# Kernel optimization log

Measured on AMD Instinct MI355X. Metric: run time of the kernel, lower is better.

Reference implementation:

```python
import math
import jax, jax.numpy as jnp
import numpy as np

B, S, E, H = 1, 2048, 2048, 16
QL, KL = 1536, 512          # q_lora_rank, kv_lora_rank
DN, DR, DV = 128, 64, 128   # qk_nope_head_dim, qk_rope_head_dim, v_head_dim
DQ = DN + DR                # q_head_dim = 192
ROPE_BASE = 10000.0
EPS = 1e-6


def _rope_cache(seq_len):
    # YaRN with scaling_factor=1.0 reduces exactly to standard RoPE (freq_extra == freq_inter,
    # mscale ratio == 1), matching DeepseekV2YarnRotaryEmbedding at default settings.
    inv_freq = 1.0 / (ROPE_BASE ** (np.arange(0, DR, 2, dtype=np.float32) / DR))
    t = np.arange(seq_len, dtype=np.float32)
    freqs = np.outer(t, inv_freq)
    emb = np.concatenate([freqs, freqs], axis=-1)  # (S, DR)
    return jnp.asarray(np.cos(emb)), jnp.asarray(np.sin(emb))


def _rmsnorm(x, w):
    return x * jax.lax.rsqrt(jnp.mean(x * x, axis=-1, keepdims=True) + EPS) * w


def _apply_rope(x, cos, sin):
    # x: (B, S, H, D). DeepseekV2 apply_rotary_pos_emb first de-interleaves
    # (view(..., d//2, 2).transpose) then uses rotate_half.
    b, s, h, d = x.shape
    xr = x.reshape(b, s, h, d // 2, 2)
    x = jnp.concatenate([xr[..., 0], xr[..., 1]], axis=-1)  # de-interleave
    rot = jnp.concatenate([-x[..., d // 2:], x[..., : d // 2]], axis=-1)
    return x * cos[None, :, None, :] + rot * sin[None, :, None, :]


def setup_inputs() -> dict:
    key = jax.random.key(0)
    ks = jax.random.split(key, 8)
    w = lambda k, shape, fan_in: (jax.random.normal(k, shape, jnp.float32) / math.sqrt(fan_in))
    return {
        "x": jax.random.normal(ks[0], (B, S, E), jnp.float32),
        "w_q_a": w(ks[1], (E, QL), E),
        "q_a_ln": jnp.ones((QL,), jnp.float32),
        "w_q_b": w(ks[2], (QL, H * DQ), QL),
        "w_kv_a": w(ks[3], (E, KL + DR), E),
        "kv_a_ln": jnp.ones((KL,), jnp.float32),
        "w_kv_b": w(ks[4], (KL, H * (DN + DV)), KL),
        "w_out": w(ks[5], (H * DV, E), H * DV),
    }


def reference(x, w_q_a, q_a_ln, w_q_b, w_kv_a, kv_a_ln, w_kv_b, w_out):
    b, s, _ = x.shape
    # Q: low-rank down-proj -> RMSNorm -> up-proj, split nope/rope parts
    q = (_rmsnorm(x @ w_q_a, q_a_ln) @ w_q_b).reshape(b, s, H, DQ)
    q_nope, q_pe = q[..., :DN], q[..., DN:]
    # KV: joint compressed latent + shared (MQA-style) rope key
    ckv = x @ w_kv_a                         # (b, s, KL+DR)
    c_kv, k_pe = ckv[..., :KL], ckv[..., KL:]
    kv = (_rmsnorm(c_kv, kv_a_ln) @ w_kv_b).reshape(b, s, H, DN + DV)
    k_nope, v = kv[..., :DN], kv[..., DN:]
    # Partial RoPE on the 64-dim rope slice only
    cos, sin = _rope_cache(s)
    q_pe = _apply_rope(q_pe, cos, sin)
    k_pe = _apply_rope(k_pe.reshape(b, s, 1, DR), cos, sin)
    qf = jnp.concatenate([q_nope, q_pe], axis=-1)                       # (b,s,H,192)
    kf = jnp.concatenate([k_nope, jnp.broadcast_to(k_pe, (b, s, H, DR))], axis=-1)
    # Causal softmax attention, scale = 1/sqrt(q_head_dim)
    scale = 1.0 / math.sqrt(DQ)
    scores = jnp.einsum("bqhd,bkhd->bhqk", qf, kf) * scale
    mask = jnp.tril(jnp.ones((s, s), dtype=bool))
    scores = jnp.where(mask[None, None], scores, jnp.finfo(scores.dtype).min)
    p = jax.nn.softmax(scores, axis=-1)
    o = jnp.einsum("bhqk,bkhd->bqhd", p, v).reshape(b, s, H * DV)
    return o @ w_out
```

## Files before the change

kernel.cpp:

```cpp
#include <hip/hip_runtime.h>
#include <hip/hip_bf16.h>
#include <math.h>

#define SS   2048
#define EE   2048
#define HH   16
#define QLAT 1536
#define KLAT 512
#define DN   128
#define DR   64
#define DV   128
#define DQ   192
#define KVD  256
#define CKVW 576
#define QW   3072
#define KVW  4096
#define OW   2048
#define QAC  2112

#define NSEG 4
#define PT_STRIDE 72
#define KTSZ (6 * 64 * 32)

typedef __attribute__((ext_vector_type(8))) short short8;
typedef __attribute__((ext_vector_type(4))) float f32x4;

__global__ void detect_dtype(const unsigned int* __restrict__ lnw, int* flag) {
    *flag = (lnw[0] == 0x3F803F80u) ? 1 : 0;
}

__device__ __forceinline__ float ld_in(const void* p, size_t i, int bf) {
    if (bf) return __bfloat162float(((const __hip_bfloat16*)p)[i]);
    return ((const float*)p)[i];
}

__device__ __forceinline__ ushort f2b(float v) {
    __hip_bfloat16 b = __float2bfloat16(v);
    return *(ushort*)&b;
}
__device__ __forceinline__ float b2f(ushort u) {
    __hip_bfloat16 b = *(__hip_bfloat16*)&u;
    return __bfloat162float(b);
}

__device__ __forceinline__ void async16(const ushort* g, ushort* l) {
    __builtin_amdgcn_global_load_lds(
        (const __attribute__((address_space(1))) void*)g,
        (__attribute__((address_space(3))) void*)l, 16, 0, 0);
}

__global__ __launch_bounds__(256) void conv_x_bf(
    const void* __restrict__ src, ushort* __restrict__ dst, int n, const int* flag) {
    const int bf = *flag;
    int i = (blockIdx.x * 256 + threadIdx.x) * 4;
    if (i >= n) return;
    ushort4 u;
    u.x = f2b(ld_in(src, i + 0, bf));
    u.y = f2b(ld_in(src, i + 1, bf));
    u.z = f2b(ld_in(src, i + 2, bf));
    u.w = f2b(ld_in(src, i + 3, bf));
    *(ushort4*)(dst + i) = u;
}

__global__ __launch_bounds__(256) void transpose_bf(
    const void* __restrict__ in, ushort* __restrict__ out,
    int R, int C, const int* flag) {
    const int bf = *flag;
    __shared__ ushort t[64][66];
    const int c0 = blockIdx.x * 64, r0 = blockIdx.y * 64;
    const int lane = threadIdx.x & 63, grp = threadIdx.x >> 6;
    #pragma unroll
    for (int p = 0; p < 16; ++p) {
        int r = p * 4 + grp;
        t[lane][r] = f2b(ld_in(in, (size_t)(r0 + r) * C + c0 + lane, bf));
    }
    __syncthreads();
    const int ro = (threadIdx.x & 31) * 2, co = threadIdx.x >> 5;
    #pragma unroll
    for (int p = 0; p < 8; ++p) {
        int c = p * 8 + co;
        ushort2 u = *(const ushort2*)&t[c][ro];
        *(ushort2*)&out[(size_t)(c0 + c) * R + r0 + ro] = u;
    }
}

__global__ __launch_bounds__(256) void gemm_bf(
    const ushort* __restrict__ A, const ushort* __restrict__ Bt,
    void* __restrict__ C, int N, int K, int lda, int ldb, int ldc,
    int cmode, const int* __restrict__ cflag) {
    __shared__ ushort As[128 * 32];
    __shared__ ushort Bs[128 * 32];
    const int tid = threadIdx.x;
    const int bm = blockIdx.y * 128, bn = blockIdx.x * 128;
    const int lane = tid & 63, wv = tid >> 6;
    const int wm = (wv & 1) * 64, wn = (wv >> 1) * 64;
    const int ln = lane & 15, quad = lane >> 4;

    f32x4 acc[4][4];
    #pragma unroll
    for (int i = 0; i < 4; ++i)
        #pragma unroll
        for (int j = 0; j < 4; ++j) acc[i][j] = (f32x4){0.f, 0.f, 0.f, 0.f};

    const int srow = tid >> 2;
    const int spart = (((tid & 3) ^ ((tid >> 3) & 3))) * 8;
    const ushort* Ag0 = A  + (size_t)(bm + srow) * lda + spart;
    const ushort* Ag1 = Ag0 + (size_t)64 * lda;
    const ushort* Bg0 = Bt + (size_t)(bn + srow) * ldb + spart;
    const ushort* Bg1 = Bg0 + (size_t)64 * ldb;
    ushort* Asl = As + tid * 8;
    ushort* Bsl = Bs + tid * 8;
    const bool bok0 = (bn + srow) < N;
    const bool bok1 = (bn + 64 + srow) < N;
    const int swq = (quad ^ ((ln >> 1) & 3)) * 8;

    for (int k0 = 0; k0 < K; k0 += 32) {
        async16(Ag0 + k0, Asl);
        async16(Ag1 + k0, Asl + 2048);
        if (bok0) async16(Bg0 + k0, Bsl);
        if (bok1) async16(Bg1 + k0, Bsl + 2048);
        __syncthreads();
        short8 af[4], bfr[4];
        #pragma unroll
        for (int t = 0; t < 4; ++t) {
            af[t]  = *(const short8*)&As[(wm + t * 16 + ln) * 32 + swq];
            bfr[t] = *(const short8*)&Bs[(wn + t * 16 + ln) * 32 + swq];
        }
        #pragma unroll
        for (int i = 0; i < 4; ++i)
            #pragma unroll
            for (int j = 0; j < 4; ++j)
                acc[i][j] = __builtin_amdgcn_mfma_f32_16x16x32_bf16(af[i], bfr[j], acc[i][j], 0, 0, 0);
        __syncthreads();
    }

    const int cbf = (cmode == 2) ? *cflag : cmode;
    #pragma unroll
    for (int i = 0; i < 4; ++i) {
        #pragma unroll
        for (int r = 0; r < 4; ++r) {
            const int m = bm + wm + i * 16 + quad * 4 + r;
            #pragma unroll
            for (int j = 0; j < 4; ++j) {
                const int n = bn + wn + j * 16 + ln;
                if (n < N) {
                    if (cbf) ((ushort*)C)[(size_t)m * ldc + n] = f2b(acc[i][j][r]);
                    else     ((float*)C)[(size_t)m * ldc + n] = acc[i][j][r];
                }
            }
        }
    }
}

__global__ __launch_bounds__(256) void gemm_bf64(
    const ushort* __restrict__ A, const ushort* __restrict__ Bt,
    void* __restrict__ C, int N, int K, int lda, int ldb, int ldc,
    int cmode, const int* __restrict__ cflag) {
    __shared__ ushort As[64 * 32];
    __shared__ ushort Bs[128 * 32];
    const int tid = threadIdx.x;
    const int bm = blockIdx.y * 64, bn = blockIdx.x * 128;
    const int lane = tid & 63, wv = tid >> 6;
    const int wm = (wv & 1) * 32, wn = (wv >> 1) * 64;
    const int ln = lane & 15, quad = lane >> 4;

    f32x4 acc[2][4];
    #pragma unroll
    for (int i = 0; i < 2; ++i)
        #pragma unroll
        for (int j = 0; j < 4; ++j) acc[i][j] = (f32x4){0.f, 0.f, 0.f, 0.f};

    const int srow = tid >> 2;
    const int spart = (((tid & 3) ^ ((tid >> 3) & 3))) * 8;
    const ushort* Ag0 = A  + (size_t)(bm + srow) * lda + spart;
    const ushort* Bg0 = Bt + (size_t)(bn + srow) * ldb + spart;
    const ushort* Bg1 = Bg0 + (size_t)64 * ldb;
    ushort* Asl = As + tid * 8;
    ushort* Bsl = Bs + tid * 8;
    const bool bok0 = (bn + srow) < N;
    const bool bok1 = (bn + 64 + srow) < N;
    const int swq = (quad ^ ((ln >> 1) & 3)) * 8;

    for (int k0 = 0; k0 < K; k0 += 32) {
        async16(Ag0 + k0, Asl);
        if (bok0) async16(Bg0 + k0, Bsl);
        if (bok1) async16(Bg1 + k0, Bsl + 2048);
        __syncthreads();
        short8 af[2], bfr[4];
        #pragma unroll
        for (int t = 0; t < 2; ++t)
            af[t] = *(const short8*)&As[(wm + t * 16 + ln) * 32 + swq];
        #pragma unroll
        for (int t = 0; t < 4; ++t)
            bfr[t] = *(const short8*)&Bs[(wn + t * 16 + ln) * 32 + swq];
        #pragma unroll
        for (int i = 0; i < 2; ++i)
            #pragma unroll
            for (int j = 0; j < 4; ++j)
                acc[i][j] = __builtin_amdgcn_mfma_f32_16x16x32_bf16(af[i], bfr[j], acc[i][j], 0, 0, 0);
        __syncthreads();
    }

    const int cbf = (cmode == 2) ? *cflag : cmode;
    #pragma unroll
    for (int i = 0; i < 2; ++i) {
        #pragma unroll
        for (int r = 0; r < 4; ++r) {
            const int m = bm + wm + i * 16 + quad * 4 + r;
            #pragma unroll
            for (int j = 0; j < 4; ++j) {
                const int n = bn + wn + j * 16 + ln;
                if (n < N) {
                    if (cbf) ((ushort*)C)[(size_t)m * ldc + n] = f2b(acc[i][j][r]);
                    else     ((float*)C)[(size_t)m * ldc + n] = acc[i][j][r];
                }
            }
        }
    }
}

__global__ __launch_bounds__(256) void rmsnorm_bf(
    ushort* __restrict__ x, const void* __restrict__ w,
    int cols, int stride, const int* wflag) {
    const int wbf = *wflag;
    ushort* p = x + (size_t)blockIdx.x * stride;
    float ss = 0.f;
    for (int i = threadIdx.x; i < cols; i += 256) { float v = b2f(p[i]); ss += v * v; }
    #pragma unroll
    for (int off = 32; off; off >>= 1) ss += __shfl_xor(ss, off);
    __shared__ float red[4];
    const int wid = threadIdx.x >> 6, lane = threadIdx.x & 63;
    if (lane == 0) red[wid] = ss;
    __syncthreads();
    const float tot = red[0] + red[1] + red[2] + red[3];
    const float scale = rsqrtf(tot / (float)cols + 1e-6f);
    for (int i = threadIdx.x; i < cols; i += 256)
        p[i] = f2b(b2f(p[i]) * scale * ld_in(w, i, wbf));
}

__device__ __forceinline__ void rope64(const float* in, float t, float* out) {
    #pragma unroll
    for (int i = 0; i < 32; ++i) {
        float inv = powf(10000.0f, -(float)i / 32.0f);
        float sv, cv;
        sincosf(t * inv, &sv, &cv);
        float x0 = in[2 * i], x1 = in[2 * i + 1];
        out[i]      = x0 * cv - x1 * sv;
        out[i + 32] = x1 * cv + x0 * sv;
    }
}

__global__ void rope_q_bf(ushort* __restrict__ q) {
    int idx = blockIdx.x * blockDim.x + threadIdx.x;
    if (idx >= SS * HH) return;
    int s = idx >> 4, h = idx & 15;
    ushort* p = q + (size_t)s * QW + h * DQ + DN;
    float buf[DR], out[DR];
    #pragma unroll
    for (int i = 0; i < DR; ++i) buf[i] = b2f(p[i]);
    rope64(buf, (float)s, out);
    #pragma unroll
    for (int i = 0; i < DR; ++i) p[i] = f2b(out[i]);
}

__global__ void rope_k_bf(const ushort* __restrict__ ckv, ushort* __restrict__ kpe,
                          int stride) {
    int s = blockIdx.x * blockDim.x + threadIdx.x;
    if (s >= SS) return;
    const ushort* p = ckv + (size_t)s * stride + KLAT;
    float buf[DR], out[DR];
    #pragma unroll
    for (int i = 0; i < DR; ++i) buf[i] = b2f(p[i]);
    rope64(buf, (float)s, out);
    ushort* dp = kpe + (size_t)s * DR;
    #pragma unroll
    for (int i = 0; i < DR; ++i) dp[i] = f2b(out[i]);
}

__global__ __launch_bounds__(256) void build_kf(
    const ushort* __restrict__ kv, const ushort* __restrict__ kpe,
    ushort* __restrict__ kf) {
    int idx = blockIdx.x * 256 + threadIdx.x;
    int part = idx % 24;
    int rest = idx / 24;
    int h = rest & 15, s = rest >> 4;
    short8 v;
    if (part < 16) v = *(const short8*)(kv + (size_t)s * KVW + h * KVD + part * 8);
    else           v = *(const short8*)(kpe + (size_t)s * DR + (part - 16) * 8);
    *(short8*)(kf + ((size_t)h * SS + s) * 192 + part * 8) = v;
}

__global__ __launch_bounds__(256) void build_vt2(
    const ushort* __restrict__ kv, ushort* __restrict__ vt2) {
    __shared__ ushort Vl[64 * 136];
    const int ck = blockIdx.x, h = blockIdx.y;
    const int tid = threadIdx.x;
    const int lane = tid & 63, wv = tid >> 6;
    #pragma unroll
    for (int rr = 0; rr < 4; ++rr) {
        int n = rr * 256 + tid;
        int key = n >> 4, part = n & 15;
        short8 v = *(const short8*)(kv + (size_t)(ck * 64 + key) * KVW + h * KVD + DN + part * 8);
        *(short8*)&Vl[key * 136 + part * 8] = v;
    }
    __syncthreads();
    const int ln = lane & 15, quad = lane >> 4;
    ushort* dst = vt2 + (((size_t)h * 32 + ck) * 16) * 512;
    #pragma unroll
    for (int w = 0; w < 4; ++w) {
        int idx2 = wv * 4 + w;
        int kb2 = idx2 >> 3, nb = idx2 & 7;
        short8 v;
        #pragma unroll
        for (int j = 0; j < 8; ++j)
            ((ushort*)&v)[j] = Vl[(kb2 * 32 + quad * 8 + j) * 136 + nb * 16 + ln];
        *(short8*)(dst + (size_t)idx2 * 512 + lane * 8) = v;
    }
}

__global__ __launch_bounds__(256, 2) void attn_mfma2(
    const ushort* __restrict__ qbf, const ushort* __restrict__ kf,
    const ushort* __restrict__ vt2, ushort* __restrict__ opart,
    float* __restrict__ ml) {
    const int seg = blockIdx.x, bq = 31 - blockIdx.y, h = blockIdx.z;
    const int ctot = bq + 1;
    const int c_lo = (seg * ctot) >> 2;
    const int nch = (((seg + 1) * ctot) >> 2) - c_lo;
    if (nch <= 0) return;

    __shared__ ushort Kt[2 * KTSZ];
    __shared__ ushort Pt[4][16 * PT_STRIDE];

    const int tid = threadIdx.x, lane = tid & 63, wl = tid >> 6;
    const int ln = lane & 15, quad = lane >> 4;
    const int qw = bq * 64 + wl * 16;
    const int kstart = c_lo << 6;
    const float scale = 0.07216878364870322f;

    short8 aq[6];
    const ushort* qrow = qbf + (size_t)(qw + ln) * QW + h * DQ;
    #pragma unroll
    for (int kb = 0; kb < 6; ++kb)
        aq[kb] = *(const short8*)(qrow + kb * 32 + quad * 8);

    const ushort* kfh = kf + (size_t)h * SS * 192;
    const ushort* vth2 = vt2 + ((size_t)h * 32 * 16) * 512 + lane * 8;

    const int key_s = tid >> 2;
    const int swp = ((tid & 3) ^ ((tid >> 3) & 3)) * 8;
    const ushort* kg = kfh + (size_t)(kstart + key_s) * 192 + swp;
    const int swq = (quad ^ ((ln >> 1) & 3)) * 8;

    f32x4 oacc[8];
    #pragma unroll
    for (int f = 0; f < 8; ++f) oacc[f] = (f32x4){0.f, 0.f, 0.f, 0.f};
    float mrow[4] = {-INFINITY, -INFINITY, -INFINITY, -INFINITY};
    float lrow[4] = {0.f, 0.f, 0.f, 0.f};

    {
        ushort* kd = Kt + tid * 8;
        #pragma unroll
        for (int i = 0; i < 6; ++i)
            async16(kg + i * 32, kd + i * 2048);
        kg += (size_t)64 * 192;
    }

    for (int c = 0; c < nch; ++c) {
        const int k0 = kstart + (c << 6);
        asm volatile("s_waitcnt vmcnt(0)" ::: "memory");
        __builtin_amdgcn_s_barrier();
        asm volatile("" ::: "memory");
        if (c + 1 < nch) {
            ushort* kd = Kt + ((c + 1) & 1) * KTSZ + tid * 8;
            #pragma unroll
            for (int i = 0; i < 6; ++i)
                async16(kg + i * 32, kd + i * 2048);
            kg += (size_t)64 * 192;
        }
        const ushort* Kcur = Kt + (c & 1) * KTSZ;

        const ushort* vfr = vth2 + (size_t)(k0 >> 6) * 16 * 512;
        short8 bv0[8];
        #pragma unroll
        for (int nb = 0; nb < 8; ++nb)
            bv0[nb] = *(const short8*)(vfr + (size_t)nb * 512);
        f32x4 s[4];
        #pragma unroll
        for (int ns = 0; ns < 4; ++ns) s[ns] = (f32x4){0.f, 0.f, 0.f, 0.f};
        __builtin_amdgcn_s_setprio(1);
        #pragma unroll
        for (int ns = 0; ns < 4; ++ns)
            #pragma unroll
            for (int kb = 0; kb < 6; ++kb) {
                short8 bk = *(const short8*)&Kcur[(kb * 64 + ns * 16 + ln) * 32 + swq];
                s[ns] = __builtin_amdgcn_mfma_f32_16x16x32_bf16(aq[kb], bk, s[ns], 0, 0, 0);
            }
        __builtin_amdgcn_s_setprio(0);
        float pv[4][4], rmax[4];
        #pragma unroll
        for (int r = 0; r < 4; ++r) rmax[r] = -1e30f;
        #pragma unroll
        for (int ns = 0; ns < 4; ++ns)
            #pragma unroll
            for (int r = 0; r < 4; ++r) {
                int key = k0 + ns * 16 + ln;
                int qr = qw + quad * 4 + r;
                float v = s[ns][r] * scale;
                if (key > qr) v = -1e30f;
                pv[ns][r] = v;
                rmax[r] = fmaxf(rmax[r], v);
            }
        #pragma unroll
        for (int off = 8; off; off >>= 1)
            #pragma unroll
            for (int r = 0; r < 4; ++r)
                rmax[r] = fmaxf(rmax[r], __shfl_xor(rmax[r], off));
        float alpha[4], psum[4];
        #pragma unroll
        for (int r = 0; r < 4; ++r) {
            float mnew = fmaxf(mrow[r], rmax[r]);
            alpha[r] = __expf(mrow[r] - mnew);
            mrow[r] = mnew;
        }
        #pragma unroll
        for (int ns = 0; ns < 4; ++ns)
            #pragma unroll
            for (int r = 0; r < 4; ++r)
                pv[ns][r] = __expf(pv[ns][r] - mrow[r]);
        #pragma unroll
        for (int r = 0; r < 4; ++r)
            psum[r] = (pv[0][r] + pv[1][r]) + (pv[2][r] + pv[3][r]);
        #pragma unroll
        for (int off = 8; off; off >>= 1)
            #pragma unroll
            for (int r = 0; r < 4; ++r)
                psum[r] += __shfl_xor(psum[r], off);
        #pragma unroll
        for (int r = 0; r < 4; ++r) lrow[r] = lrow[r] * alpha[r] + psum[r];
        #pragma unroll
        for (int f = 0; f < 8; ++f)
            #pragma unroll
            for (int r = 0; r < 4; ++r) oacc[f][r] *= alpha[r];
        #pragma unroll
        for (int ns = 0; ns < 4; ++ns)
            #pragma unroll
            for (int r = 0; r < 4; ++r)
                Pt[wl][(quad * 4 + r) * PT_STRIDE + ns * 16 + ln] = f2b(pv[ns][r]);
        short8 bv1[8];
        #pragma unroll
        for (int nb = 0; nb < 8; ++nb)
            bv1[nb] = *(const short8*)(vfr + (size_t)(8 + nb) * 512);
        short8 pa0 = *(const short8*)&Pt[wl][ln * PT_STRIDE + quad * 8];
        short8 pa1 = *(const short8*)&Pt[wl][ln * PT_STRIDE + 32 + quad * 8];
        __builtin_amdgcn_s_setprio(1);
        #pragma unroll
        for (int nb = 0; nb < 8; ++nb)
            oacc[nb] = __builtin_amdgcn_mfma_f32_16x16x32_bf16(pa0, bv0[nb], oacc[nb], 0, 0, 0);
        #pragma unroll
        for (int nb = 0; nb < 8; ++nb)
            oacc[nb] = __builtin_amdgcn_mfma_f32_16x16x32_bf16(pa1, bv1[nb], oacc[nb], 0, 0, 0);
        __builtin_amdgcn_s_setprio(0);
    }

    const size_t pbase = (((size_t)h * 32 + bq) * NSEG + seg) * 64;
    #pragma unroll
    for (int nb = 0; nb < 8; ++nb)
        #pragma unroll
        for (int r = 0; r < 4; ++r)
            opart[(pbase + wl * 16 + quad * 4 + r) * 128 + nb * 16 + ln] = f2b(oacc[nb][r]);
    if (ln == 0) {
        #pragma unroll
        for (int r = 0; r < 4; ++r) {
            ml[(pbase + wl * 16 + quad * 4 + r) * 2]     = mrow[r];
            ml[(pbase + wl * 16 + quad * 4 + r) * 2 + 1] = lrow[r];
        }
    }
}

__global__ __launch_bounds__(256) void merge_attn(
    const ushort* __restrict__ opart, const float* __restrict__ ml,
    ushort* __restrict__ obf) {
    const int q = blockIdx.x;
    const int bq = q >> 6, row = q & 63;
    const int ctot = bq + 1;
    const int t = threadIdx.x;
    #pragma unroll
    for (int pp = 0; pp < 8; ++pp) {
        int idx = pp * 256 + t;
        int h = idx >> 7, d = idx & 127;
        size_t rbase = (((size_t)h * 32 + bq) * NSEG) * 64 + row;
        float M = -1e30f;
        #pragma unroll
        for (int s = 0; s < NSEG; ++s) {
            if ((((s + 1) * ctot) >> 2) > ((s * ctot) >> 2))
                M = fmaxf(M, ml[(rbase + (size_t)s * 64) * 2]);
        }
        float L = 0.f, acc = 0.f;
        #pragma unroll
        for (int s = 0; s < NSEG; ++s) {
            if ((((s + 1) * ctot) >> 2) > ((s * ctot) >> 2)) {
                size_t ri = rbase + (size_t)s * 64;
                float w = __expf(ml[ri * 2] - M);
                L += w * ml[ri * 2 + 1];
                acc += w * b2f(opart[ri * 128 + d]);
            }
        }
        obf[(size_t)q * OW + h * DV + d] = f2b(acc / L);
    }
}

extern "C" void kernel_launch(void* const* d_in, const int* in_sizes, int n_in,
                              void* d_out, int out_size, void* d_ws, size_t ws_size,
                              hipStream_t stream) {
    const void* x       = d_in[0];
    const void* w_q_a   = d_in[1];
    const void* q_a_ln  = d_in[2];
    const void* w_q_b   = d_in[3];
    const void* w_kv_a  = d_in[4];
    const void* kv_a_ln = d_in[5];
    const void* w_kv_b  = d_in[6];
    const void* w_out   = d_in[7];

    char* ws = (char*)d_ws;
    int*    flag  = (int*)ws;
    ushort* qbf   = (ushort*)(ws + 256);
    ushort* obf   = qbf   + (size_t)SS * QW;
    ushort* wqat  = obf   + (size_t)SS * OW;
    ushort* wkvat = wqat  + (size_t)QLAT * EE;
    ushort* wqbt  = wkvat + (size_t)CKVW * EE;
    ushort* wkvbt = wqbt  + (size_t)QW * QLAT;
    ushort* woutt = wkvbt + (size_t)KVW * KLAT;
    ushort* kf    = woutt + (size_t)EE * OW;
    ushort* vt2   = kf    + (size_t)HH * SS * 192;
    float*  ml    = (float*)(vt2 + (size_t)HH * SS * DV);
    ushort* qac   = (ushort*)(ml + (size_t)HH * 32 * NSEG * 64 * 2);
    ushort* xbf   = qac   + (size_t)SS * QAC;
    ushort* kvbf  = xbf   + (size_t)SS * EE;
    ushort* kpebf = kvbf  + (size_t)SS * KVW;
    ushort* opart = qac;

    detect_dtype<<<1, 1, 0, stream>>>((const unsigned int*)q_a_ln, flag);

    conv_x_bf<<<(SS * EE / 4 + 255) / 256, 256, 0, stream>>>(x, xbf, SS * EE, flag);
    transpose_bf<<<dim3(QLAT / 64, EE / 64), 256, 0, stream>>>(w_q_a, wqat, EE, QLAT, flag);
    transpose_bf<<<dim3(CKVW / 64, EE / 64), 256, 0, stream>>>(w_kv_a, wkvat, EE, CKVW, flag);
    transpose_bf<<<dim3(QW / 64, QLAT / 64), 256, 0, stream>>>(w_q_b, wqbt, QLAT, QW, flag);
    transpose_bf<<<dim3(KVW / 64, KLAT / 64), 256, 0, stream>>>(w_kv_b, wkvbt, KLAT, KVW, flag);
    transpose_bf<<<dim3(EE / 64, OW / 64), 256, 0, stream>>>(w_out, woutt, OW, EE, flag);

    gemm_bf64<<<dim3((QAC + 127) / 128, SS / 64), 256, 0, stream>>>(
        xbf, wqat, qac, QAC, EE, EE, EE, QAC, 1, nullptr);

    rmsnorm_bf<<<SS, 256, 0, stream>>>(qac, q_a_ln, QLAT, QAC, flag);
    rmsnorm_bf<<<SS, 256, 0, stream>>>(qac + QLAT, kv_a_ln, KLAT, QAC, flag);

    gemm_bf<<<dim3(QW / 128, SS / 128), 256, 0, stream>>>(
        qac, wqbt, qbf, QW, QLAT, QAC, QLAT, QW, 1, nullptr);
    gemm_bf<<<dim3(KVW / 128, SS / 128), 256, 0, stream>>>(
        qac + QLAT, wkvbt, kvbf, KVW, KLAT, QAC, KLAT, KVW, 1, nullptr);

    rope_q_bf<<<(SS * HH + 255) / 256, 256, 0, stream>>>(qbf);
    rope_k_bf<<<(SS + 63) / 64, 64, 0, stream>>>(qac + QLAT, kpebf, QAC);

    build_kf<<<SS * HH * 24 / 256, 256, 0, stream>>>(kvbf, kpebf, kf);
    build_vt2<<<dim3(SS / 64, HH), 256, 0, stream>>>(kvbf, vt2);

    attn_mfma2<<<dim3(NSEG, SS / 64, HH), 256, 0, stream>>>(qbf, kf, vt2, opart, ml);
    merge_attn<<<SS, 256, 0, stream>>>(opart, ml, obf);

    gemm_bf64<<<dim3(EE / 128, SS / 64), 256, 0, stream>>>(
        obf, woutt, d_out, EE, OW, OW, OW, EE, 2, flag);
}
```

Before: 440.8 us.

## Double-buffer GEMM LDS loads and merge transpose, rmsnorm and rope launches

Both bf16 MFMA GEMM kernels now use two LDS buffers. The async global-to-LDS loads for the next K-step are issued while MFMAs run on the current step, which removes one barrier per iteration and raises wave priority around the MFMA block. Separately, the five weight-transpose launches are merged into one 3D-grid kernel, the two RMSNorm launches into one, and the q/k RoPE launches into one, to cut launch overhead. The trade-off is doubled LDS per GEMM block, which may lower occupancy, plus some idle blocks in the merged transpose grid.

```diff
diff --git a/kernel.cpp b/kernel.cpp
--- a/kernel.cpp
+++ b/kernel.cpp
@@ -62,12 +62,26 @@
     *(ushort4*)(dst + i) = u;
 }
 
-__global__ __launch_bounds__(256) void transpose_bf(
-    const void* __restrict__ in, ushort* __restrict__ out,
-    int R, int C, const int* flag) {
+__global__ __launch_bounds__(256) void transpose5_bf(
+    const void* __restrict__ s0, const void* __restrict__ s1,
+    const void* __restrict__ s2, const void* __restrict__ s3,
+    const void* __restrict__ s4,
+    ushort* __restrict__ d0, ushort* __restrict__ d1, ushort* __restrict__ d2,
+    ushort* __restrict__ d3, ushort* __restrict__ d4,
+    const int* flag) {
+    const int z = blockIdx.z;
+    const void* in; ushort* out; int R, C;
+    switch (z) {
+        case 0:  in = s0; out = d0; R = EE;   C = QLAT; break;
+        case 1:  in = s1; out = d1; R = EE;   C = CKVW; break;
+        case 2:  in = s2; out = d2; R = QLAT; C = QW;   break;
+        case 3:  in = s3; out = d3; R = KLAT; C = KVW;  break;
+        default: in = s4; out = d4; R = OW;   C = EE;   break;
+    }
+    const int c0 = blockIdx.x * 64, r0 = blockIdx.y * 64;
+    if (c0 >= C || r0 >= R) return;
     const int bf = *flag;
     __shared__ ushort t[64][66];
-    const int c0 = blockIdx.x * 64, r0 = blockIdx.y * 64;
     const int lane = threadIdx.x & 63, grp = threadIdx.x >> 6;
     #pragma unroll
     for (int p = 0; p < 16; ++p) {
@@ -88,8 +102,8 @@
     const ushort* __restrict__ A, const ushort* __restrict__ Bt,
     void* __restrict__ C, int N, int K, int lda, int ldb, int ldc,
     int cmode, const int* __restrict__ cflag) {
-    __shared__ ushort As[128 * 32];
-    __shared__ ushort Bs[128 * 32];
+    __shared__ ushort As[2][128 * 32];
+    __shared__ ushort Bs[2][128 * 32];
     const int tid = threadIdx.x;
     const int bm = blockIdx.y * 128, bn = blockIdx.x * 128;
     const int lane = tid & 63, wv = tid >> 6;
@@ -108,30 +122,49 @@
     const ushort* Ag1 = Ag0 + (size_t)64 * lda;
     const ushort* Bg0 = Bt + (size_t)(bn + srow) * ldb + spart;
     const ushort* Bg1 = Bg0 + (size_t)64 * ldb;
-    ushort* Asl = As + tid * 8;
-    ushort* Bsl = Bs + tid * 8;
     const bool bok0 = (bn + srow) < N;
     const bool bok1 = (bn + 64 + srow) < N;
     const int swq = (quad ^ ((ln >> 1) & 3)) * 8;
-
-    for (int k0 = 0; k0 < K; k0 += 32) {
-        async16(Ag0 + k0, Asl);
-        async16(Ag1 + k0, Asl + 2048);
-        if (bok0) async16(Bg0 + k0, Bsl);
-        if (bok1) async16(Bg1 + k0, Bsl + 2048);
-        __syncthreads();
+    const int nsteps = K >> 5;
+
+    {
+        ushort* Asl = As[0] + tid * 8;
+        ushort* Bsl = Bs[0] + tid * 8;
+        async16(Ag0, Asl);
+        async16(Ag1, Asl + 2048);
+        if (bok0) async16(Bg0, Bsl);
+        if (bok1) async16(Bg1, Bsl + 2048);
+    }
+
+    for (int c = 0; c < nsteps; ++c) {
+        asm volatile("s_waitcnt vmcnt(0)" ::: "memory");
+        __builtin_amdgcn_s_barrier();
+        asm volatile("" ::: "memory");
+        if (c + 1 < nsteps) {
+            const int k1 = (c + 1) << 5;
+            const int nb = (c + 1) & 1;
+            ushort* Asl = As[nb] + tid * 8;
+            ushort* Bsl = Bs[nb] + tid * 8;
+            async16(Ag0 + k1, Asl);
+            async16(Ag1 + k1, Asl + 2048);
+            if (bok0) async16(Bg0 + k1, Bsl);
+            if (bok1) async16(Bg1 + k1, Bsl + 2048);
+        }
+        const ushort* Ac = As[c & 1];
+        const ushort* Bc = Bs[c & 1];
         short8 af[4], bfr[4];
         #pragma unroll
         for (int t = 0; t < 4; ++t) {
-            af[t]  = *(const short8*)&As[(wm + t * 16 + ln) * 32 + swq];
-            bfr[t] = *(const short8*)&Bs[(wn + t * 16 + ln) * 32 + swq];
-        }
+            af[t]  = *(const short8*)&Ac[(wm + t * 16 + ln) * 32 + swq];
+            bfr[t] = *(const short8*)&Bc[(wn + t * 16 + ln) * 32 + swq];
+        }
+        __builtin_amdgcn_s_setprio(1);
         #pragma unroll
         for (int i = 0; i < 4; ++i)
             #pragma unroll
             for (int j = 0; j < 4; ++j)
                 acc[i][j] = __builtin_amdgcn_mfma_f32_16x16x32_bf16(af[i], bfr[j], acc[i][j], 0, 0, 0);
-        __syncthreads();
+        __builtin_amdgcn_s_setprio(0);
     }
 
     const int cbf = (cmode == 2) ? *cflag : cmode;
@@ -156,8 +189,8 @@
     const ushort* __restrict__ A, const ushort* __restrict__ Bt,
     void* __restrict__ C, int N, int K, int lda, int ldb, int ldc,
     int cmode, const int* __restrict__ cflag) {
-    __shared__ ushort As[64 * 32];
-    __shared__ ushort Bs[128 * 32];
+    __shared__ ushort As[2][64 * 32];
+    __shared__ ushort Bs[2][128 * 32];
     const int tid = threadIdx.x;
     const int bm = blockIdx.y * 64, bn = blockIdx.x * 128;
     const int lane = tid & 63, wv = tid >> 6;
@@ -175,30 +208,48 @@
     const ushort* Ag0 = A  + (size_t)(bm + srow) * lda + spart;
     const ushort* Bg0 = Bt + (size_t)(bn + srow) * ldb + spart;
     const ushort* Bg1 = Bg0 + (size_t)64 * ldb;
-    ushort* Asl = As + tid * 8;
-    ushort* Bsl = Bs + tid * 8;
     const bool bok0 = (bn + srow) < N;
     const bool bok1 = (bn + 64 + srow) < N;
     const int swq = (quad ^ ((ln >> 1) & 3)) * 8;
-
-    for (int k0 = 0; k0 < K; k0 += 32) {
-        async16(Ag0 + k0, Asl);
-        if (bok0) async16(Bg0 + k0, Bsl);
-        if (bok1) async16(Bg1 + k0, Bsl + 2048);
-        __syncthreads();
+    const int nsteps = K >> 5;
+
+    {
+        ushort* Asl = As[0] + tid * 8;
+        ushort* Bsl = Bs[0] + tid * 8;
+        async16(Ag0, Asl);
+        if (bok0) async16(Bg0, Bsl);
+        if (bok1) async16(Bg1, Bsl + 2048);
+    }
+
+    for (int c = 0; c < nsteps; ++c) {
+        asm volatile("s_waitcnt vmcnt(0)" ::: "memory");
+        __builtin_amdgcn_s_barrier();
+        asm volatile("" ::: "memory");
+        if (c + 1 < nsteps) {
+            const int k1 = (c + 1) << 5;
+            const int nb = (c + 1) & 1;
+            ushort* Asl = As[nb] + tid * 8;
+            ushort* Bsl = Bs[nb] + tid * 8;
+            async16(Ag0 + k1, Asl);
+            if (bok0) async16(Bg0 + k1, Bsl);
+            if (bok1) async16(Bg1 + k1, Bsl + 2048);
+        }
+        const ushort* Ac = As[c & 1];
+        const ushort* Bc = Bs[c & 1];
         short8 af[2], bfr[4];
         #pragma unroll
         for (int t = 0; t < 2; ++t)
-            af[t] = *(const short8*)&As[(wm + t * 16 + ln) * 32 + swq];
+            af[t] = *(const short8*)&Ac[(wm + t * 16 + ln) * 32 + swq];
         #pragma unroll
         for (int t = 0; t < 4; ++t)
-            bfr[t] = *(const short8*)&Bs[(wn + t * 16 + ln) * 32 + swq];
+            bfr[t] = *(const short8*)&Bc[(wn + t * 16 + ln) * 32 + swq];
+        __builtin_amdgcn_s_setprio(1);
         #pragma unroll
         for (int i = 0; i < 2; ++i)
             #pragma unroll
             for (int j = 0; j < 4; ++j)
                 acc[i][j] = __builtin_amdgcn_mfma_f32_16x16x32_bf16(af[i], bfr[j], acc[i][j], 0, 0, 0);
-        __syncthreads();
+        __builtin_amdgcn_s_setprio(0);
     }
 
     const int cbf = (cmode == 2) ? *cflag : cmode;
@@ -219,11 +270,14 @@
     }
 }
 
-__global__ __launch_bounds__(256) void rmsnorm_bf(
-    ushort* __restrict__ x, const void* __restrict__ w,
-    int cols, int stride, const int* wflag) {
+__global__ __launch_bounds__(256) void rmsnorm2_bf(
+    ushort* __restrict__ x, const void* __restrict__ wq,
+    const void* __restrict__ wkv, const int* wflag) {
     const int wbf = *wflag;
-    ushort* p = x + (size_t)blockIdx.x * stride;
+    const int which = blockIdx.y;
+    const int cols = which ? KLAT : QLAT;
+    const void* w = which ? wkv : wq;
+    ushort* p = x + (size_t)blockIdx.x * QAC + (which ? QLAT : 0);
     float ss = 0.f;
     for (int i = threadIdx.x; i < cols; i += 256) { float v = b2f(p[i]); ss += v * v; }
     #pragma unroll
@@ -250,31 +304,29 @@
     }
 }
 
-__global__ void rope_q_bf(ushort* __restrict__ q) {
+__global__ void rope_all_bf(ushort* __restrict__ q, const ushort* __restrict__ qac,
+                            ushort* __restrict__ kpe) {
     int idx = blockIdx.x * blockDim.x + threadIdx.x;
-    if (idx >= SS * HH) return;
-    int s = idx >> 4, h = idx & 15;
-    ushort* p = q + (size_t)s * QW + h * DQ + DN;
-    float buf[DR], out[DR];
-    #pragma unroll
-    for (int i = 0; i < DR; ++i) buf[i] = b2f(p[i]);
-    rope64(buf, (float)s, out);
-    #pragma unroll
-    for (int i = 0; i < DR; ++i) p[i] = f2b(out[i]);
-}
-
-__global__ void rope_k_bf(const ushort* __restrict__ ckv, ushort* __restrict__ kpe,
-                          int stride) {
-    int s = blockIdx.x * blockDim.x + threadIdx.x;
-    if (s >= SS) return;
-    const ushort* p = ckv + (size_t)s * stride + KLAT;
-    float buf[DR], out[DR];
-    #pragma unroll
-    for (int i = 0; i < DR; ++i) buf[i] = b2f(p[i]);
-    rope64(buf, (float)s, out);
-    ushort* dp = kpe + (size_t)s * DR;
-    #pragma unroll
-    for (int i = 0; i < DR; ++i) dp[i] = f2b(out[i]);
+    if (idx < SS * HH) {
+        int s = idx >> 4, h = idx & 15;
+        ushort* p = q + (size_t)s * QW + h * DQ + DN;
+        float buf[DR], out[DR];
+        #pragma unroll
+        for (int i = 0; i < DR; ++i) buf[i] = b2f(p[i]);
+        rope64(buf, (float)s, out);
+        #pragma unroll
+        for (int i = 0; i < DR; ++i) p[i] = f2b(out[i]);
+    } else if (idx < SS * HH + SS) {
+        int s = idx - SS * HH;
+        const ushort* p = qac + (size_t)s * QAC + QLAT + KLAT;
+        float buf[DR], out[DR];
+        #pragma unroll
+        for (int i = 0; i < DR; ++i) buf[i] = b2f(p[i]);
+        rope64(buf, (float)s, out);
+        ushort* dp = kpe + (size_t)s * DR;
+        #pragma unroll
+        for (int i = 0; i < DR; ++i) dp[i] = f2b(out[i]);
+    }
 }
 
 __global__ __launch_bounds__(256) void build_kf(
@@ -542,25 +594,21 @@
     detect_dtype<<<1, 1, 0, stream>>>((const unsigned int*)q_a_ln, flag);
 
     conv_x_bf<<<(SS * EE / 4 + 255) / 256, 256, 0, stream>>>(x, xbf, SS * EE, flag);
-    transpose_bf<<<dim3(QLAT / 64, EE / 64), 256, 0, stream>>>(w_q_a, wqat, EE, QLAT, flag);
-    transpose_bf<<<dim3(CKVW / 64, EE / 64), 256, 0, stream>>>(w_kv_a, wkvat, EE, CKVW, flag);
-    transpose_bf<<<dim3(QW / 64, QLAT / 64), 256, 0, stream>>>(w_q_b, wqbt, QLAT, QW, flag);
-    transpose_bf<<<dim3(KVW / 64, KLAT / 64), 256, 0, stream>>>(w_kv_b, wkvbt, KLAT, KVW, flag);
-    transpose_bf<<<dim3(EE / 64, OW / 64), 256, 0, stream>>>(w_out, woutt, OW, EE, flag);
+    transpose5_bf<<<dim3(64, 32, 5), 256, 0, stream>>>(
+        w_q_a, w_kv_a, w_q_b, w_kv_b, w_out,
+        wqat, wkvat, wqbt, wkvbt, woutt, flag);
 
     gemm_bf64<<<dim3((QAC + 127) / 128, SS / 64), 256, 0, stream>>>(
         xbf, wqat, qac, QAC, EE, EE, EE, QAC, 1, nullptr);
 
-    rmsnorm_bf<<<SS, 256, 0, stream>>>(qac, q_a_ln, QLAT, QAC, flag);
-    rmsnorm_bf<<<SS, 256, 0, stream>>>(qac + QLAT, kv_a_ln, KLAT, QAC, flag);
+    rmsnorm2_bf<<<dim3(SS, 2), 256, 0, stream>>>(qac, q_a_ln, kv_a_ln, flag);
 
     gemm_bf<<<dim3(QW / 128, SS / 128), 256, 0, stream>>>(
         qac, wqbt, qbf, QW, QLAT, QAC, QLAT, QW, 1, nullptr);
     gemm_bf<<<dim3(KVW / 128, SS / 128), 256, 0, stream>>>(
         qac + QLAT, wkvbt, kvbf, KVW, KLAT, QAC, KLAT, KVW, 1, nullptr);
 
-    rope_q_bf<<<(SS * HH + 255) / 256, 256, 0, stream>>>(qbf);
-    rope_k_bf<<<(SS + 63) / 64, 64, 0, stream>>>(qac + QLAT, kpebf, QAC);
+    rope_all_bf<<<(SS * HH + SS + 255) / 256, 256, 0, stream>>>(qbf, qac, kpebf);
 
     build_kf<<<SS * HH * 24 / 256, 256, 0, stream>>>(kvbf, kpebf, kf);
     build_vt2<<<dim3(SS / 64, HH), 256, 0, stream>>>(kvbf, vt2);
```

Measured after the change: 417.3 us. 1.06x faster.
